# Kernel tuning notes

Measured on AMD Instinct MI355X. Metric: run time of the kernel, lower is better.

## Reference

```python
import jax, jax.numpy as jnp
import numpy as np

N, E = 10000, 160000
F_IN, H1, C1, C2 = 256, 8, 128, 128
SLOPE = 0.2  # PyG GATConv default negative_slope


def setup_inputs() -> dict:
    key = jax.random.key(0)
    ks = jax.random.split(key, 9)
    s = 0.05
    return {
        "x": jax.random.normal(ks[0], (N, F_IN), jnp.float32),
        "edge_index": jax.random.randint(ks[1], (2, E), 0, N),
        "W1": jax.random.normal(ks[2], (F_IN, H1 * C1), jnp.float32) * s,
        "a_src1": jax.random.normal(ks[3], (H1, C1), jnp.float32) * s,
        "a_dst1": jax.random.normal(ks[4], (H1, C1), jnp.float32) * s,
        "b1": jnp.zeros((H1 * C1,), jnp.float32),
        "W2": jax.random.normal(ks[5], (H1 * C1, C2), jnp.float32) * s,
        "a_src2": jax.random.normal(ks[6], (1, C2), jnp.float32) * s,
        "a_dst2": jax.random.normal(ks[7], (1, C2), jnp.float32) * s,
        "b2": jnp.zeros((C2,), jnp.float32),
    }


def gat_conv(x, src, dst, W, a_s, a_d, b, heads, out_ch, concat):
    n = x.shape[0]
    h = (x @ W).reshape(n, heads, out_ch)            # [N,H,C]
    s_src = jnp.einsum("nhc,hc->nh", h, a_s)         # [N,H]
    s_dst = jnp.einsum("nhc,hc->nh", h, a_d)
    e = jax.nn.leaky_relu(s_src[src] + s_dst[dst], SLOPE)   # [Etot,H]
    # segment softmax over incoming edges per destination (self-loops guarantee non-empty segments)
    m = jax.lax.stop_gradient(jax.ops.segment_max(e, dst, num_segments=n))
    p = jnp.exp(e - m[dst])
    denom = jax.ops.segment_sum(p, dst, num_segments=n)
    alpha = p / denom[dst]                            # [Etot,H]
    out = jax.ops.segment_sum(h[src] * alpha[:, :, None], dst, num_segments=n)  # [N,H,C]
    out = out.reshape(n, heads * out_ch) if concat else out.mean(axis=1)
    return out + b


def reference(x, edge_index, W1, a_src1, a_dst1, b1, W2, a_src2, a_dst2, b2):
    n = x.shape[0]
    loops = jnp.arange(n, dtype=edge_index.dtype)     # PyG add_self_loops=True
    src = jnp.concatenate([edge_index[0], loops])
    dst = jnp.concatenate([edge_index[1], loops])
    # dropout layers are identity at inference (training=False)
    h1 = jax.nn.elu(gat_conv(x, src, dst, W1, a_src1, a_dst1, b1, H1, C1, True))
    return gat_conv(h1, src, dst, W2, a_src2, a_dst2, b2, 1, C2, False)
```

## Files before the change

kernel.cpp:

```cpp
#include <hip/hip_runtime.h>
#include <math.h>

#define F_IN 256
#define H1 8
#define C1 128
#define HC1 1024
#define C2 128
#define SLOPE 0.2f

typedef unsigned short u16;
typedef __attribute__((ext_vector_type(8))) short bf16x8;
typedef __attribute__((ext_vector_type(4))) float f32x4;


__device__ __forceinline__ float lrelu(float v) { return v > 0.f ? v : SLOPE * v; }

__device__ __forceinline__ unsigned bf16_rne(float x) {
    unsigned u = __float_as_uint(x);
    u += 0x7fffu + ((u >> 16) & 1u);
    return u >> 16;
}

__device__ __forceinline__ void split2(float a, float b, unsigned& hi, unsigned& lo) {
    unsigned ha = bf16_rne(a), hb = bf16_rne(b);
    float fa = __uint_as_float(ha << 16), fb = __uint_as_float(hb << 16);
    hi = ha | (hb << 16);
    lo = bf16_rne(a - fa) | (bf16_rne(b - fb) << 16);
}

__device__ __forceinline__ void gload16(const u16* g, u16* l) {
    __builtin_amdgcn_global_load_lds(
        (const __attribute__((address_space(1))) unsigned*)g,
        (__attribute__((address_space(3))) unsigned*)l, 16, 0, 0);
}


__global__ void init_deg(int* deg, int n) {
    int i = blockIdx.x * blockDim.x + threadIdx.x;
    if (i < n) deg[i] = 1;
}

__global__ void hist_kernel(const int* __restrict__ dst, int* __restrict__ deg, int E) {
    int i = blockIdx.x * blockDim.x + threadIdx.x;
    if (i < E) atomicAdd(&deg[dst[i]], 1);
}

__global__ void scan_kernel(const int* __restrict__ deg, int* __restrict__ start,
                            int* __restrict__ cursor, int n) {
    __shared__ int buf[1024];
    int carry = 0;
    for (int base = 0; base < n; base += 1024) {
        int i = base + (int)threadIdx.x;
        int v = (i < n) ? deg[i] : 0;
        buf[threadIdx.x] = v;
        __syncthreads();
        for (int offd = 1; offd < 1024; offd <<= 1) {
            int tv = 0;
            if ((int)threadIdx.x >= offd) tv = buf[threadIdx.x - offd];
            __syncthreads();
            if ((int)threadIdx.x >= offd) buf[threadIdx.x] += tv;
            __syncthreads();
        }
        int incl = buf[threadIdx.x];
        if (i < n) { start[i] = carry + incl - v; cursor[i] = carry + incl - v; }
        carry += buf[1023];
        __syncthreads();
    }
    if (threadIdx.x == 0) start[n] = carry;
}

__global__ void scatter_kernel(const int* __restrict__ src, const int* __restrict__ dst,
                               int* __restrict__ cursor, int* __restrict__ ssorted,
                               int E, int N) {
    int i = blockIdx.x * blockDim.x + threadIdx.x;
    if (i < E) {
        int d = dst[i];
        int pos = atomicAdd(&cursor[d], 1);
        ssorted[pos] = src[i];
    } else if (i < E + N) {
        int d = i - E;
        int pos = atomicAdd(&cursor[d], 1);
        ssorted[pos] = d;
    }
}


__global__ void split_mat(const float* __restrict__ in, u16* __restrict__ hi,
                          u16* __restrict__ lo, int n) {
    int i = blockIdx.x * blockDim.x + threadIdx.x;
    if (i >= n) return;
    float v = in[i];
    unsigned h = bf16_rne(v);
    hi[i] = (u16)h;
    lo[i] = (u16)bf16_rne(v - __uint_as_float(h << 16));
}

__global__ void split_transpose(const float* __restrict__ in, u16* __restrict__ hi,
                                u16* __restrict__ lo, int R, int C) {
    int i = blockIdx.x * blockDim.x + threadIdx.x;
    if (i >= R * C) return;
    int r = i / C, c = i % C;
    float v = in[i];
    unsigned h = bf16_rne(v);
    hi[(size_t)c * R + r] = (u16)h;
    lo[(size_t)c * R + r] = (u16)bf16_rne(v - __uint_as_float(h << 16));
}


__global__ __launch_bounds__(256) void gemm_mfma(const u16* __restrict__ Ahi,
                                                 const u16* __restrict__ Alo,
                                                 const u16* __restrict__ Bhi,
                                                 const u16* __restrict__ Blo,
                                                 u16* __restrict__ Cbf,
                                                 int M, int N, int K) {
    __shared__ u16 lds[16384];
    const int t = threadIdx.x;
    const int rbase = blockIdx.y * 128;
    const int cbase = blockIdx.x * 128;

    const int lane = t & 63;
    const int R0 = (t >> 7) << 6;
    const int C0 = ((t >> 6) & 1) << 6;
    const int lrow = lane & 15;
    const int kq = lane >> 4;

    f32x4 acc[4][4] = {};

    for (int k0 = 0; k0 < K; k0 += 32) {
#pragma unroll
        for (int i = 0; i < 2; i++) {
            int c = t + (i << 8);
            int row = c >> 2;
            int kc = (c & 3) << 3;
            int ar = min(rbase + row, M - 1);
            int br = cbase + row;
            gload16(Ahi + (size_t)ar * K + k0 + kc, &lds[c * 8]);
            gload16(Alo + (size_t)ar * K + k0 + kc, &lds[4096 + c * 8]);
            gload16(Bhi + (size_t)br * K + k0 + kc, &lds[8192 + c * 8]);
            gload16(Blo + (size_t)br * K + k0 + kc, &lds[12288 + c * 8]);
        }
        __syncthreads();

        bf16x8 ah[4], al[4], bh[4], bl[4];
#pragma unroll
        for (int m = 0; m < 4; m++) {
            int off = (R0 + (m << 4) + lrow) * 32 + (kq << 3);
            ah[m] = *(const bf16x8*)&lds[off];
            al[m] = *(const bf16x8*)&lds[4096 + off];
        }
#pragma unroll
        for (int n = 0; n < 4; n++) {
            int off = (C0 + (n << 4) + lrow) * 32 + (kq << 3);
            bh[n] = *(const bf16x8*)&lds[8192 + off];
            bl[n] = *(const bf16x8*)&lds[12288 + off];
        }
#pragma unroll
        for (int m = 0; m < 4; m++)
#pragma unroll
            for (int n = 0; n < 4; n++) {
                acc[m][n] = __builtin_amdgcn_mfma_f32_16x16x32_bf16(ah[m], bh[n], acc[m][n], 0, 0, 0);
                acc[m][n] = __builtin_amdgcn_mfma_f32_16x16x32_bf16(ah[m], bl[n], acc[m][n], 0, 0, 0);
                acc[m][n] = __builtin_amdgcn_mfma_f32_16x16x32_bf16(al[m], bh[n], acc[m][n], 0, 0, 0);
            }
        __syncthreads();
    }

#pragma unroll
    for (int m = 0; m < 4; m++)
#pragma unroll
        for (int n = 0; n < 4; n++) {
            int col = cbase + C0 + (n << 4) + lrow;
#pragma unroll
            for (int r = 0; r < 4; r++) {
                int row = rbase + R0 + (m << 4) + kq * 4 + r;
                if (row < M) Cbf[(size_t)row * N + col] = (u16)bf16_rne(acc[m][n][r]);
            }
        }
}


__global__ __launch_bounds__(256) void gemm_mfma64(const u16* __restrict__ Ahi,
                                                   const u16* __restrict__ Alo,
                                                   const u16* __restrict__ Bhi,
                                                   const u16* __restrict__ Blo,
                                                   u16* __restrict__ Cbf,
                                                   int M, int N, int K) {
    __shared__ u16 lds[8192];
    const int t = threadIdx.x;
    const int rbase = blockIdx.y * 64;
    const int cbase = blockIdx.x * 64;

    const int lane = t & 63;
    const int w = t >> 6;
    const int R0 = (w >> 1) << 5;
    const int C0 = (w & 1) << 5;
    const int lrow = lane & 15;
    const int kq = lane >> 4;

    f32x4 acc[2][2] = {};

    for (int k0 = 0; k0 < K; k0 += 32) {
        {
            int row = t >> 2;
            int kc = (t & 3) << 3;
            int ar = min(rbase + row, M - 1);
            int br = cbase + row;
            gload16(Ahi + (size_t)ar * K + k0 + kc, &lds[t * 8]);
            gload16(Alo + (size_t)ar * K + k0 + kc, &lds[2048 + t * 8]);
            gload16(Bhi + (size_t)br * K + k0 + kc, &lds[4096 + t * 8]);
            gload16(Blo + (size_t)br * K + k0 + kc, &lds[6144 + t * 8]);
        }
        __syncthreads();

        bf16x8 ah[2], al[2], bh[2], bl[2];
#pragma unroll
        for (int m = 0; m < 2; m++) {
            int off = (R0 + (m << 4) + lrow) * 32 + (kq << 3);
            ah[m] = *(const bf16x8*)&lds[off];
            al[m] = *(const bf16x8*)&lds[2048 + off];
        }
#pragma unroll
        for (int n = 0; n < 2; n++) {
            int off = (C0 + (n << 4) + lrow) * 32 + (kq << 3);
            bh[n] = *(const bf16x8*)&lds[4096 + off];
            bl[n] = *(const bf16x8*)&lds[6144 + off];
        }
#pragma unroll
        for (int m = 0; m < 2; m++)
#pragma unroll
            for (int n = 0; n < 2; n++) {
                acc[m][n] = __builtin_amdgcn_mfma_f32_16x16x32_bf16(ah[m], bh[n], acc[m][n], 0, 0, 0);
                acc[m][n] = __builtin_amdgcn_mfma_f32_16x16x32_bf16(ah[m], bl[n], acc[m][n], 0, 0, 0);
                acc[m][n] = __builtin_amdgcn_mfma_f32_16x16x32_bf16(al[m], bh[n], acc[m][n], 0, 0, 0);
            }
        __syncthreads();
    }

#pragma unroll
    for (int m = 0; m < 2; m++)
#pragma unroll
        for (int n = 0; n < 2; n++) {
            int col = cbase + C0 + (n << 4) + lrow;
#pragma unroll
            for (int r = 0; r < 4; r++) {
                int row = rbase + R0 + (m << 4) + kq * 4 + r;
                if (row < M) Cbf[(size_t)row * N + col] = (u16)bf16_rne(acc[m][n][r]);
            }
        }
}


__global__ __launch_bounds__(256) void scores1_bf(const unsigned* __restrict__ hbf,
                                                  const float* __restrict__ a_s,
                                                  const float* __restrict__ a_d,
                                                  float* __restrict__ ssrc,
                                                  float* __restrict__ sdst, int N) {
    int wid = blockIdx.x * 4 + (threadIdx.x >> 6);
    if (wid >= N * H1) return;
    int lane = threadIdx.x & 63;
    int n = wid >> 3, hh = wid & 7;
    unsigned u = hbf[(size_t)n * 512 + hh * 64 + lane];
    float c0 = __uint_as_float(u << 16);
    float c1 = __uint_as_float(u & 0xffff0000u);
    const float* as = a_s + hh * C1;
    const float* ad = a_d + hh * C1;
    float vs = c0 * as[2 * lane] + c1 * as[2 * lane + 1];
    float vd = c0 * ad[2 * lane] + c1 * ad[2 * lane + 1];
    for (int off = 32; off; off >>= 1) {
        vs += __shfl_xor(vs, off);
        vd += __shfl_xor(vd, off);
    }
    if (lane == 0) { ssrc[wid] = vs; sdst[wid] = vd; }
}

__global__ __launch_bounds__(256) void scores2_bf(const unsigned* __restrict__ hbf,
                                                  const float* __restrict__ a_s,
                                                  const float* __restrict__ a_d,
                                                  float* __restrict__ ssrc,
                                                  float* __restrict__ sdst, int N) {
    int n = blockIdx.x * 4 + (threadIdx.x >> 6);
    if (n >= N) return;
    int lane = threadIdx.x & 63;
    unsigned u = hbf[(size_t)n * 64 + lane];
    float c0 = __uint_as_float(u << 16);
    float c1 = __uint_as_float(u & 0xffff0000u);
    float vs = c0 * a_s[2 * lane] + c1 * a_s[2 * lane + 1];
    float vd = c0 * a_d[2 * lane] + c1 * a_d[2 * lane + 1];
    for (int off = 32; off; off >>= 1) {
        vs += __shfl_xor(vs, off);
        vd += __shfl_xor(vd, off);
    }
    if (lane == 0) { ssrc[n] = vs; sdst[n] = vd; }
}


template<int H, bool SPLITOUT>
__global__ __launch_bounds__(256) void agg_bf(const unsigned* __restrict__ hbf,
                                              const float* __restrict__ ssrc,
                                              const float* __restrict__ sdst,
                                              const int* __restrict__ start,
                                              const int* __restrict__ ssorted,
                                              const float* __restrict__ bias,
                                              float* __restrict__ out,
                                              unsigned* __restrict__ outHi,
                                              unsigned* __restrict__ outLo, int N) {
    int hh, grp;
    if (H == 8) { hh = blockIdx.x & 7; grp = blockIdx.x >> 3; }
    else        { hh = 0;              grp = blockIdx.x; }
    int wid = threadIdx.x >> 6, lane = threadIdx.x & 63;
    int d = grp * 4 + wid;
    if (d >= N) return;
    const int g = lane >> 4, p = lane & 15;
    int s0 = start[d];
    int ne = start[d + 1] - s0;
    float sd = sdst[d * H + hh];

    const unsigned* hlane = hbf + hh * 64 + p * 4;
    const int rowstride = H * 64;

    int src0 = 0; float v0 = -1e30f;
    if (lane < ne) { src0 = ssorted[s0 + lane]; v0 = lrelu(ssrc[src0 * H + hh] + sd); }
    float m = v0;
    for (int e = lane + 64; e < ne; e += 64)
        m = fmaxf(m, lrelu(ssrc[ssorted[s0 + e] * H + hh] + sd));
    for (int o = 32; o; o >>= 1) m = fmaxf(m, __shfl_xor(m, o));

    float p0 = (lane < ne) ? __expf(v0 - m) : 0.f;
    float ssum = p0;
    for (int e = lane + 64; e < ne; e += 64)
        ssum += __expf(lrelu(ssrc[ssorted[s0 + e] * H + hh] + sd) - m);
    for (int o = 32; o; o >>= 1) ssum += __shfl_xor(ssum, o);
    float inv = 1.f / ssum;

    float acc[8] = {};
    for (int base = 0; base < ne; base += 64) {
        int srcr; float al;
        if (base == 0) { srcr = src0; al = p0 * inv; }
        else {
            srcr = 0; al = 0.f;
            int e = base + lane;
            if (e < ne) {
                srcr = ssorted[s0 + e];
                al = __expf(lrelu(ssrc[srcr * H + hh] + sd) - m) * inv;
            }
        }
        int cnt = min(64, ne - base);
        for (int e2 = 0; e2 < cnt; e2 += 4) {
            float a = __shfl(al, e2 + g);
            int sr = __shfl(srcr, e2 + g);
            uint4 u = *(const uint4*)(hlane + (size_t)sr * rowstride);
            acc[0] += a * __uint_as_float(u.x << 16);
            acc[1] += a * __uint_as_float(u.x & 0xffff0000u);
            acc[2] += a * __uint_as_float(u.y << 16);
            acc[3] += a * __uint_as_float(u.y & 0xffff0000u);
            acc[4] += a * __uint_as_float(u.z << 16);
            acc[5] += a * __uint_as_float(u.z & 0xffff0000u);
            acc[6] += a * __uint_as_float(u.w << 16);
            acc[7] += a * __uint_as_float(u.w & 0xffff0000u);
        }
    }

#pragma unroll
    for (int i = 0; i < 8; i++) {
        acc[i] += __shfl_xor(acc[i], 16);
        acc[i] += __shfl_xor(acc[i], 32);
    }

    float r0 = g == 0 ? acc[0] : g == 1 ? acc[2] : g == 2 ? acc[4] : acc[6];
    float r1 = g == 0 ? acc[1] : g == 1 ? acc[3] : g == 2 ? acc[5] : acc[7];
    int j = 4 * p + g;
    float2 bv = ((const float2*)bias)[hh * 64 + j];
    r0 += bv.x; r1 += bv.y;
    size_t idx = (size_t)d * (H * 64) + hh * 64 + j;
    if (SPLITOUT) {
        r0 = r0 > 0.f ? r0 : expm1f(r0);
        r1 = r1 > 0.f ? r1 : expm1f(r1);
        unsigned hi, lo;
        split2(r0, r1, hi, lo);
        outHi[idx] = hi;
        outLo[idx] = lo;
    } else {
        ((float2*)out)[idx] = make_float2(r0, r1);
    }
}


extern "C" void kernel_launch(void* const* d_in, const int* in_sizes, int n_in,
                              void* d_out, int out_size, void* d_ws, size_t ws_size,
                              hipStream_t stream) {
    const float* x      = (const float*)d_in[0];
    const int*   ei     = (const int*)d_in[1];
    const float* W1     = (const float*)d_in[2];
    const float* a_src1 = (const float*)d_in[3];
    const float* a_dst1 = (const float*)d_in[4];
    const float* b1     = (const float*)d_in[5];
    const float* W2     = (const float*)d_in[6];
    const float* a_src2 = (const float*)d_in[7];
    const float* a_dst2 = (const float*)d_in[8];
    const float* b2     = (const float*)d_in[9];
    float* out = (float*)d_out;

    int E = in_sizes[1] / 2;
    int N = in_sizes[0] / F_IN;
    const int* esrc = ei;
    const int* edst = ei + E;

    char* ws = (char*)d_ws;
    size_t off = 0;
    auto alloc = [&](size_t bytes) -> char* {
        char* p = ws + off;
        off = (off + bytes + 255) & ~(size_t)255;
        return p;
    };
    u16* x_hi    = (u16*)alloc((size_t)N * F_IN * 2);
    u16* x_lo    = (u16*)alloc((size_t)N * F_IN * 2);
    u16* W1t_hi  = (u16*)alloc((size_t)F_IN * HC1 * 2);
    u16* W1t_lo  = (u16*)alloc((size_t)F_IN * HC1 * 2);
    u16* W2t_hi  = (u16*)alloc((size_t)HC1 * C2 * 2);
    u16* W2t_lo  = (u16*)alloc((size_t)HC1 * C2 * 2);
    u16* h1_bf   = (u16*)alloc((size_t)N * HC1 * 2);
    u16* h1a_hi  = (u16*)alloc((size_t)N * HC1 * 2);
    u16* h1a_lo  = (u16*)alloc((size_t)N * HC1 * 2);
    u16* h2_bf   = (u16*)alloc((size_t)N * C2 * 2);
    float* ss1   = (float*)alloc((size_t)N * H1 * 4);
    float* sd1   = (float*)alloc((size_t)N * H1 * 4);
    float* ss2   = (float*)alloc((size_t)N * 4);
    float* sd2   = (float*)alloc((size_t)N * 4);
    int* deg     = (int*)alloc((size_t)N * 4);
    int* startp  = (int*)alloc((size_t)(N + 1) * 4);
    int* cursor  = (int*)alloc((size_t)N * 4);
    int* ssorted = (int*)alloc((size_t)(E + N) * 4);

    init_deg<<<(N + 255) / 256, 256, 0, stream>>>(deg, N);
    hist_kernel<<<(E + 255) / 256, 256, 0, stream>>>(edst, deg, E);
    scan_kernel<<<1, 1024, 0, stream>>>(deg, startp, cursor, N);
    scatter_kernel<<<(E + N + 255) / 256, 256, 0, stream>>>(esrc, edst, cursor, ssorted, E, N);

    split_mat<<<(N * F_IN + 255) / 256, 256, 0, stream>>>(x, x_hi, x_lo, N * F_IN);
    split_transpose<<<(F_IN * HC1 + 255) / 256, 256, 0, stream>>>(W1, W1t_hi, W1t_lo, F_IN, HC1);
    split_transpose<<<(HC1 * C2 + 255) / 256, 256, 0, stream>>>(W2, W2t_hi, W2t_lo, HC1, C2);

    gemm_mfma<<<dim3(HC1 / 128, (N + 127) / 128), 256, 0, stream>>>(
        x_hi, x_lo, W1t_hi, W1t_lo, h1_bf, N, HC1, F_IN);
    scores1_bf<<<(N * H1 + 3) / 4, 256, 0, stream>>>(
        (const unsigned*)h1_bf, a_src1, a_dst1, ss1, sd1, N);
    agg_bf<H1, true><<<((N + 3) / 4) * H1, 256, 0, stream>>>(
        (const unsigned*)h1_bf, ss1, sd1, startp, ssorted, b1,
        nullptr, (unsigned*)h1a_hi, (unsigned*)h1a_lo, N);

    gemm_mfma64<<<dim3(C2 / 64, (N + 63) / 64), 256, 0, stream>>>(
        h1a_hi, h1a_lo, W2t_hi, W2t_lo, h2_bf, N, C2, HC1);
    scores2_bf<<<(N + 3) / 4, 256, 0, stream>>>(
        (const unsigned*)h2_bf, a_src2, a_dst2, ss2, sd2, N);
    agg_bf<1, false><<<(N + 3) / 4, 256, 0, stream>>>(
        (const unsigned*)h2_bf, ss2, sd2, startp, ssorted, b2,
        out, nullptr, nullptr, N);
}
```

Baseline: 258.1 us.

## Split layer-1 aggregation into edge softmax pass and MFMA sparse aggregation

Layer-1 attention aggregation is split into two kernels. The first computes per-edge softmax coefficients per head into a buffer that reuses the x_hi workspace. The second aggregates 16 destination rows per block by building a one-hot-masked alpha matrix (hi/lo bf16 split) and running MFMA against gathered source features. This aims to replace the scalar per-wave gather-accumulate with matrix-core work, at the cost of an extra edge pass, a global alpha round trip, byte-wide row-location tags written during scatter, and wasted MFMA lanes on the masked rows.

```diff
diff --git a/kernel.cpp b/kernel.cpp
--- a/kernel.cpp
+++ b/kernel.cpp
@@ -71,16 +71,19 @@
 
 __global__ void scatter_kernel(const int* __restrict__ src, const int* __restrict__ dst,
                                int* __restrict__ cursor, int* __restrict__ ssorted,
+                               unsigned char* __restrict__ rowloc,
                                int E, int N) {
     int i = blockIdx.x * blockDim.x + threadIdx.x;
     if (i < E) {
         int d = dst[i];
         int pos = atomicAdd(&cursor[d], 1);
         ssorted[pos] = src[i];
+        rowloc[pos] = (unsigned char)(d & 15);
     } else if (i < E + N) {
         int d = i - E;
         int pos = atomicAdd(&cursor[d], 1);
         ssorted[pos] = d;
+        rowloc[pos] = (unsigned char)(d & 15);
     }
 }
 
@@ -291,6 +294,133 @@
         vd += __shfl_xor(vd, off);
     }
     if (lane == 0) { ssrc[n] = vs; sdst[n] = vd; }
+}
+
+
+__global__ __launch_bounds__(256) void softmax_edges1(
+    const float* __restrict__ ssrc, const float* __restrict__ sdst,
+    const int* __restrict__ start, const int* __restrict__ ssorted,
+    float* __restrict__ alphab, int N, int ET) {
+    int lane = threadIdx.x & 63;
+    int p = lane & 15, g = lane >> 4;
+    int task = (blockIdx.x * 4 + (threadIdx.x >> 6)) * 4 + g;
+    if (task >= N * H1) return;
+    int d = task >> 3, hh = task & 7;
+    int s0 = start[d], ne = start[d + 1] - s0;
+    float sd = sdst[d * H1 + hh];
+    int src0 = 0; float v0 = -1e30f;
+    if (p < ne) { src0 = ssorted[s0 + p]; v0 = lrelu(ssrc[src0 * H1 + hh] + sd); }
+    float m = v0;
+    for (int e = p + 16; e < ne; e += 16)
+        m = fmaxf(m, lrelu(ssrc[ssorted[s0 + e] * H1 + hh] + sd));
+    for (int o = 8; o; o >>= 1) m = fmaxf(m, __shfl_xor(m, o));
+    float p0 = (p < ne) ? __expf(v0 - m) : 0.f;
+    float s = p0;
+    for (int e = p + 16; e < ne; e += 16)
+        s += __expf(lrelu(ssrc[ssorted[s0 + e] * H1 + hh] + sd) - m);
+    for (int o = 8; o; o >>= 1) s += __shfl_xor(s, o);
+    float inv = 1.f / s;
+    float* ab = alphab + (size_t)hh * ET;
+    if (p < ne) ab[s0 + p] = p0 * inv;
+    for (int e = p + 16; e < ne; e += 16)
+        ab[s0 + e] = __expf(lrelu(ssrc[ssorted[s0 + e] * H1 + hh] + sd) - m) * inv;
+}
+
+
+__global__ __launch_bounds__(256) void agg_mfma1(
+    const u16* __restrict__ hbf,
+    const float* __restrict__ alphab,
+    const unsigned char* __restrict__ rowloc,
+    const int* __restrict__ start,
+    const int* __restrict__ ssorted,
+    const float* __restrict__ bias,
+    u16* __restrict__ outHi, u16* __restrict__ outLo,
+    int N, int ET) {
+    __shared__ unsigned mAl[32];
+    __shared__ int mSrc[32];
+    __shared__ unsigned mRow[32];
+
+    const int hh = blockIdx.x & 7;
+    const int g = blockIdx.x >> 3;
+    const int t = threadIdx.x;
+    const int w = t >> 6;
+    const int lane = t & 63;
+    const int cl = lane & 15, q = lane >> 4;
+
+    const int d0 = g * 16;
+    const int e0 = start[d0], e1 = start[min(d0 + 16, N)];
+    const float* ab = alphab + (size_t)hh * ET;
+
+    const int n0 = w * 2;
+    const u16* hcol = hbf + (size_t)hh * C1 + n0 * 16 + cl;
+
+    f32x4 acc0 = {}, acc1 = {};
+
+    for (int kb = e0; kb < e1; kb += 32) {
+        __syncthreads();
+        if (t < 32) {
+            int pos = kb + t;
+            bool valid = pos < e1;
+            int ps = valid ? pos : e0;
+            float af = valid ? ab[ps] : 0.f;
+            unsigned ahiu = bf16_rne(af);
+            unsigned alou = bf16_rne(af - __uint_as_float(ahiu << 16));
+            mAl[t] = ahiu | (alou << 16);
+            mSrc[t] = ssorted[ps];
+            mRow[t] = rowloc[ps];
+        }
+        __syncthreads();
+
+        uint4 ma0 = *(const uint4*)&mAl[q * 8];
+        uint4 ma1 = *(const uint4*)&mAl[q * 8 + 4];
+        uint4 mr0 = *(const uint4*)&mRow[q * 8];
+        uint4 mr1 = *(const uint4*)&mRow[q * 8 + 4];
+        int4  ms0 = *(const int4*)&mSrc[q * 8];
+        int4  ms1 = *(const int4*)&mSrc[q * 8 + 4];
+        unsigned mm[8] = {ma0.x, ma0.y, ma0.z, ma0.w, ma1.x, ma1.y, ma1.z, ma1.w};
+        unsigned rr[8] = {mr0.x, mr0.y, mr0.z, mr0.w, mr1.x, mr1.y, mr1.z, mr1.w};
+        int      ss[8] = {ms0.x, ms0.y, ms0.z, ms0.w, ms1.x, ms1.y, ms1.z, ms1.w};
+
+        bf16x8 ahi, alo;
+#pragma unroll
+        for (int j = 0; j < 8; j++) {
+            bool mt = (int)rr[j] == cl;
+            ahi[j] = mt ? (short)(mm[j] & 0xffffu) : (short)0;
+            alo[j] = mt ? (short)(mm[j] >> 16) : (short)0;
+        }
+
+        bf16x8 b0, b1;
+#pragma unroll
+        for (int j = 0; j < 8; j++) {
+            const u16* pj = hcol + ((size_t)ss[j] << 10);
+            b0[j] = (short)pj[0];
+            b1[j] = (short)pj[16];
+        }
+
+        acc0 = __builtin_amdgcn_mfma_f32_16x16x32_bf16(ahi, b0, acc0, 0, 0, 0);
+        acc0 = __builtin_amdgcn_mfma_f32_16x16x32_bf16(alo, b0, acc0, 0, 0, 0);
+        acc1 = __builtin_amdgcn_mfma_f32_16x16x32_bf16(ahi, b1, acc1, 0, 0, 0);
+        acc1 = __builtin_amdgcn_mfma_f32_16x16x32_bf16(alo, b1, acc1, 0, 0, 0);
+    }
+
+#pragma unroll
+    for (int nn = 0; nn < 2; nn++) {
+        f32x4 a = nn ? acc1 : acc0;
+        int ch = (n0 + nn) * 16 + cl;
+        float bv = bias[hh * C1 + ch];
+#pragma unroll
+        for (int r = 0; r < 4; r++) {
+            int d = d0 + q * 4 + r;
+            if (d >= N) continue;
+            float v = a[r] + bv;
+            v = v > 0.f ? v : expm1f(v);
+            unsigned hi = bf16_rne(v);
+            unsigned lo = bf16_rne(v - __uint_as_float(hi << 16));
+            size_t idx = (size_t)d * HC1 + hh * C1 + ch;
+            outHi[idx] = (u16)hi;
+            outLo[idx] = (u16)lo;
+        }
+    }
 }
 
 
@@ -402,6 +532,7 @@
 
     int E = in_sizes[1] / 2;
     int N = in_sizes[0] / F_IN;
+    int ET = E + N;
     const int* esrc = ei;
     const int* edst = ei + E;
 
@@ -429,12 +560,14 @@
     int* deg     = (int*)alloc((size_t)N * 4);
     int* startp  = (int*)alloc((size_t)(N + 1) * 4);
     int* cursor  = (int*)alloc((size_t)N * 4);
-    int* ssorted = (int*)alloc((size_t)(E + N) * 4);
+    int* ssorted = (int*)alloc((size_t)ET * 4);
+    unsigned char* rowloc = (unsigned char*)alloc((size_t)ET);
+    float* alpha1 = (float*)x_hi;
 
     init_deg<<<(N + 255) / 256, 256, 0, stream>>>(deg, N);
     hist_kernel<<<(E + 255) / 256, 256, 0, stream>>>(edst, deg, E);
     scan_kernel<<<1, 1024, 0, stream>>>(deg, startp, cursor, N);
-    scatter_kernel<<<(E + N + 255) / 256, 256, 0, stream>>>(esrc, edst, cursor, ssorted, E, N);
+    scatter_kernel<<<(E + N + 255) / 256, 256, 0, stream>>>(esrc, edst, cursor, ssorted, rowloc, E, N);
 
     split_mat<<<(N * F_IN + 255) / 256, 256, 0, stream>>>(x, x_hi, x_lo, N * F_IN);
     split_transpose<<<(F_IN * HC1 + 255) / 256, 256, 0, stream>>>(W1, W1t_hi, W1t_lo, F_IN, HC1);
@@ -444,9 +577,10 @@
         x_hi, x_lo, W1t_hi, W1t_lo, h1_bf, N, HC1, F_IN);
     scores1_bf<<<(N * H1 + 3) / 4, 256, 0, stream>>>(
         (const unsigned*)h1_bf, a_src1, a_dst1, ss1, sd1, N);
-    agg_bf<H1, true><<<((N + 3) / 4) * H1, 256, 0, stream>>>(
-        (const unsigned*)h1_bf, ss1, sd1, startp, ssorted, b1,
-        nullptr, (unsigned*)h1a_hi, (unsigned*)h1a_lo, N);
+    softmax_edges1<<<(N * H1 + 15) / 16, 256, 0, stream>>>(
+        ss1, sd1, startp, ssorted, alpha1, N, ET);
+    agg_mfma1<<<((N + 15) / 16) * H1, 256, 0, stream>>>(
+        h1_bf, alpha1, rowloc, startp, ssorted, b1, h1a_hi, h1a_lo, N, ET);
 
     gemm_mfma64<<<dim3(C2 / 64, (N + 63) / 64), 256, 0, stream>>>(
         h1a_hi, h1a_lo, W2t_hi, W2t_lo, h2_bf, N, C2, HC1);
```

Result: slower. 265.8 us (+3.0%).
